# Optimization experiments

Measured on AMD Instinct MI355X. Metric: run time of the kernel, lower is better.

The kernel has to match this reference:

```python
import jax, jax.numpy as jnp
import numpy as np

N, D, C = 2048, 192, 100000
S, M = 30.0, 0.2

def setup_inputs() -> dict:
    key = jax.random.key(0)
    k1, k2, k3 = jax.random.split(key, 3)
    x = jax.random.normal(k1, (N, D), dtype=jnp.float32)
    W = jax.random.normal(k2, (C, D), dtype=jnp.float32) * 0.05
    label = jax.random.randint(k3, (N,), 0, C, dtype=jnp.int64)
    return {"x": x, "W": W, "label": label}

def reference(x, W, label):
    # NOTE: the original torch code's weight-normalization loop is a no-op
    # (it rebinds the local name W, never mutating the parameter), so W is
    # intentionally NOT normalized here; only x is.
    xn = x / jnp.linalg.norm(x, axis=1, keepdims=True)          # [N, D]
    wf = jnp.einsum("nd,cd->nc", xn, W)                          # [N, C]
    tgt = jnp.take_along_axis(wf, label[:, None], axis=1)[:, 0]  # [N]
    numer = S * (tgt - M)                                        # margin-adjusted target logit
    logits = S * wf
    # replace the label column with the margin-adjusted numerator so that
    # logsumexp(logits) == log(exp(numer) + sum_{j!=y} exp(s*wf[:,j]))
    logits = logits.at[jnp.arange(N), label].set(numer)
    L = numer - jax.nn.logsumexp(logits, axis=1)                 # [N]
    return -jnp.mean(L)
```

## Files before the change

### kernel.cpp

```cpp
#include <hip/hip_runtime.h>
#include <stdint.h>


constexpr int N  = 2048;
constexpr int D  = 192;
constexpr int C  = 100000;
constexpr int KT = D / 32;
constexpr int TILE = 512;
constexpr int RT16 = C / 16;
constexpr int TPG = 12;
constexpr int CX = 523;
constexpr int NT16 = CX * TPG;
constexpr float PHANTOM = (float)(NT16 * 16 - C);
constexpr int BANDS = 4;
constexpr int RYB = N / (64 * BANDS);
constexpr int BUF = 4 * KT * TILE;
constexpr int NXB = N / 4;

#define S_SCALE 30.0f
#define MARGIN  0.2f
#define S_LOG2E 43.2808512266689f

using short8 = __attribute__((ext_vector_type(8))) short;
using f32x4  = __attribute__((ext_vector_type(4))) float;

typedef __attribute__((address_space(1))) const void GV;
typedef __attribute__((address_space(3))) void LV;

__device__ inline unsigned short f2bf(float f) {
  unsigned int u = __float_as_uint(f);
  u += 0x7fffu + ((u >> 16) & 1u);
  return (unsigned short)(u >> 16);
}

__device__ inline int pack_idx(int r, int k) {
  return ((r >> 4) * KT + (k >> 5)) * TILE + (((k >> 3) & 3) * 16 + (r & 15)) * 8 + (k & 7);
}

__device__ inline float row_sum16(float v) {
  int x;
  x = __float_as_int(v);
  v += __int_as_float(__builtin_amdgcn_update_dpp(0, x, 0x128, 0xF, 0xF, true));
  x = __float_as_int(v);
  v += __int_as_float(__builtin_amdgcn_update_dpp(0, x, 0x124, 0xF, 0xF, true));
  x = __float_as_int(v);
  v += __int_as_float(__builtin_amdgcn_update_dpp(0, x, 0x04E, 0xF, 0xF, true));
  x = __float_as_int(v);
  v += __int_as_float(__builtin_amdgcn_update_dpp(0, x, 0x0B1, 0xF, 0xF, true));
  return v;
}

__global__ __launch_bounds__(256) void prep_all(
    const float* __restrict__ x, const float* __restrict__ W,
    unsigned short* __restrict__ xnb, unsigned short* __restrict__ Wb,
    float* __restrict__ out) {
  const int bid  = blockIdx.x;
  const int lane = threadIdx.x & 63;
  if (bid == 0 && threadIdx.x == 0) out[0] = 0.0f;

  if (bid < NXB) {
    const int row = bid * 4 + (threadIdx.x >> 6);
    const float* xr = x + (size_t)row * D;
    float v0 = xr[lane], v1 = xr[lane + 64], v2 = xr[lane + 128];
    float ss = v0 * v0 + v1 * v1 + v2 * v2;
#pragma unroll
    for (int off = 32; off > 0; off >>= 1) ss += __shfl_xor(ss, off, 64);
    const float inv = rsqrtf(ss) * S_LOG2E;
    xnb[pack_idx(row, lane)]       = f2bf(v0 * inv);
    xnb[pack_idx(row, lane + 64)]  = f2bf(v1 * inv);
    xnb[pack_idx(row, lane + 128)] = f2bf(v2 * inv);
  } else {
    const int t16 = (bid - NXB) * 4 + (threadIdx.x >> 6);
    const int m = lane & 15, q = lane >> 4;
    unsigned short* dst = Wb + (size_t)t16 * KT * TILE + lane * 8;
    if (t16 < RT16) {
      const float* src = W + (size_t)(t16 * 16 + m) * D + q * 8;
#pragma unroll
      for (int ks = 0; ks < KT; ++ks) {
        const float4* s4 = (const float4*)(src + ks * 32);
        float4 f0 = s4[0], f1 = s4[1];
        short8 hv;
        hv[0] = (short)f2bf(f0.x); hv[1] = (short)f2bf(f0.y);
        hv[2] = (short)f2bf(f0.z); hv[3] = (short)f2bf(f0.w);
        hv[4] = (short)f2bf(f1.x); hv[5] = (short)f2bf(f1.y);
        hv[6] = (short)f2bf(f1.z); hv[7] = (short)f2bf(f1.w);
        *(short8*)(dst + (size_t)ks * TILE) = hv;
      }
    } else {
      const short8 z = {0, 0, 0, 0, 0, 0, 0, 0};
#pragma unroll
      for (int ks = 0; ks < KT; ++ks) *(short8*)(dst + (size_t)ks * TILE) = z;
    }
  }
}

__global__ __launch_bounds__(256, 3) void gemm_lse(
    const unsigned short* __restrict__ xnb,
    const unsigned short* __restrict__ Wb,
    float* __restrict__ partial) {
  __shared__ alignas(16) unsigned short As[2 * BUF];
  __shared__ alignas(16) float rs_lds[4][256];

  const int tid = threadIdx.x;
  const int bid = blockIdx.x;
  const int cx = bid >> 3, ry = bid & 7;

  {
    const unsigned short* slab = xnb + (size_t)(ry * BANDS) * BUF;
#pragma unroll
    for (int i = 0; i < 6; ++i) {
      const int chunk = tid + i * 256;
      __builtin_amdgcn_global_load_lds(
          (GV*)((const char*)slab + (size_t)chunk * 16),
          (LV*)((char*)As + (size_t)chunk * 16), 16, 0, 0);
    }
  }

  const int lane = tid & 63, wave = tid >> 6;
  const int m = lane & 15, quad = lane >> 4;

  short8 breg[3][KT];
#pragma unroll
  for (int tc = 0; tc < 3; ++tc)
#pragma unroll
    for (int ks = 0; ks < KT; ++ks)
      breg[tc][ks] = *(const short8*)(
          Wb + (size_t)((cx * TPG + wave * 3 + tc) * KT + ks) * TILE + lane * 8);

  const f32x4 zero4 = {0.0f, 0.0f, 0.0f, 0.0f};

  for (int b = 0; b < BANDS; ++b) {
    __syncthreads();

    if (b + 1 < BANDS) {
      const unsigned short* slab = xnb + (size_t)(ry * BANDS + b + 1) * BUF;
      char* dst = (char*)&As[((b + 1) & 1) * BUF];
#pragma unroll
      for (int i = 0; i < 6; ++i) {
        const int chunk = tid + i * 256;
        __builtin_amdgcn_global_load_lds(
            (GV*)((const char*)slab + (size_t)chunk * 16),
            (LV*)(dst + (size_t)chunk * 16), 16, 0, 0);
      }
    }

    const unsigned short* Ab = &As[(b & 1) * BUF];

    f32x4 acc[4][3];
#pragma unroll
    for (int a = 0; a < 4; ++a)
#pragma unroll
      for (int c = 0; c < 3; ++c) acc[a][c] = zero4;

#pragma unroll
    for (int ks = 0; ks < KT; ++ks) {
      short8 af[4];
#pragma unroll
      for (int tr = 0; tr < 4; ++tr)
        af[tr] = *(const short8*)(&Ab[(tr * KT + ks) * TILE + lane * 8]);
#pragma unroll
      for (int tr = 0; tr < 4; ++tr)
#pragma unroll
        for (int tc = 0; tc < 3; ++tc)
          acc[tr][tc] = __builtin_amdgcn_mfma_f32_16x16x32_bf16(
              af[tr], breg[tc][ks], acc[tr][tc], 0, 0, 0);
    }

#pragma unroll
    for (int tr = 0; tr < 4; ++tr) {
      float rv0 = 0.f, rv1 = 0.f, rv2 = 0.f, rv3 = 0.f;
#pragma unroll
      for (int tc = 0; tc < 3; ++tc) {
        rv0 += __builtin_amdgcn_exp2f(acc[tr][tc][0]);
        rv1 += __builtin_amdgcn_exp2f(acc[tr][tc][1]);
        rv2 += __builtin_amdgcn_exp2f(acc[tr][tc][2]);
        rv3 += __builtin_amdgcn_exp2f(acc[tr][tc][3]);
      }
      rv0 = row_sum16(rv0);
      rv1 = row_sum16(rv1);
      rv2 = row_sum16(rv2);
      rv3 = row_sum16(rv3);
      if (m == 0) {
        float4 v = make_float4(rv0, rv1, rv2, rv3);
        *(float4*)(&rs_lds[wave][b * 64 + tr * 16 + quad * 4]) = v;
      }
    }
  }

  __syncthreads();
  if (tid < 256) {
    const float s = rs_lds[0][tid] + rs_lds[1][tid] + rs_lds[2][tid] + rs_lds[3][tid];
    partial[(size_t)cx * N + ry * 256 + tid] = s;
  }
}

__global__ __launch_bounds__(256) void finalize_rows(
    const float* __restrict__ x, const float* __restrict__ W,
    const int* __restrict__ label, const float* __restrict__ partial,
    float* __restrict__ out) {
  const int row  = blockIdx.x * 4 + (threadIdx.x >> 6);
  const int lane = threadIdx.x & 63;
  const float* xr = x + (size_t)row * D;
  float v0 = xr[lane], v1 = xr[lane + 64], v2 = xr[lane + 128];
  float ss = v0 * v0 + v1 * v1 + v2 * v2;
  const int lab = label[row];
  const float* wr = W + (size_t)lab * D;
  float d = v0 * wr[lane] + v1 * wr[lane + 64] + v2 * wr[lane + 128];
  float p = 0.0f;
  for (int s = lane; s < CX; s += 64) p += partial[(size_t)s * N + row];
#pragma unroll
  for (int off = 32; off > 0; off >>= 1) {
    ss += __shfl_xor(ss, off, 64);
    d  += __shfl_xor(d,  off, 64);
    p  += __shfl_xor(p,  off, 64);
  }
  __shared__ float part[4];
  if (lane == 0) {
    const float tgt   = d * rsqrtf(ss);
    const float numer = S_SCALE * (tgt - MARGIN);
    const float se = p - PHANTOM - __expf(S_SCALE * tgt) + __expf(numer);
    part[threadIdx.x >> 6] = numer - logf(se);
  }
  __syncthreads();
  if (threadIdx.x == 0) {
    const float blocksum = part[0] + part[1] + part[2] + part[3];
    atomicAdd(out, -blocksum * (1.0f / (float)N));
  }
}

extern "C" void kernel_launch(void* const* d_in, const int* in_sizes, int n_in,
                              void* d_out, int out_size, void* d_ws, size_t ws_size,
                              hipStream_t stream) {
  const float* x     = (const float*)d_in[0];
  const float* W     = (const float*)d_in[1];
  const int*   label = (const int*)d_in[2];
  float*       out   = (float*)d_out;

  char* ws = (char*)d_ws;
  size_t off = 0;
  unsigned short* xnb = (unsigned short*)(ws + off); off += (size_t)N * D * 2;
  unsigned short* Wb  = (unsigned short*)(ws + off); off += (size_t)NT16 * KT * TILE * 2;
  float* partial = (float*)(ws + off); off += (size_t)CX * N * 4;

  prep_all<<<NXB + NT16 / 4, 256, 0, stream>>>(x, W, xnb, Wb, out);

  gemm_lse<<<CX * RYB, 256, 0, stream>>>(xnb, Wb, partial);

  finalize_rows<<<N / 4, 256, 0, stream>>>(x, W, label, partial, out);
}
```

Before: 211.5 us.

## Fuse W bf16 conversion into GEMM kernel, dropping packed W workspace

Removes the W-conversion half of the prep kernel and the packed bf16 W buffer. Each GEMM block now loads its fp32 W rows directly into registers and converts them to bf16 in the MFMA fragment layout, zero-filling phantom tiles. This avoids writing the bf16 copy of W and reading it back. The cost is that each W tile is fetched in fp32 (twice the bytes) by all 8 row-band blocks, which relies on L2/MALL reuse among adjacent blocks, and the conversion is repeated in each of those blocks.

```diff
diff --git a/kernel.cpp b/kernel.cpp
--- a/kernel.cpp
+++ b/kernel.cpp
@@ -50,31 +50,56 @@
   return v;
 }
 
-__global__ __launch_bounds__(256) void prep_all(
-    const float* __restrict__ x, const float* __restrict__ W,
-    unsigned short* __restrict__ xnb, unsigned short* __restrict__ Wb,
+__global__ __launch_bounds__(256) void prep_x(
+    const float* __restrict__ x, unsigned short* __restrict__ xnb,
     float* __restrict__ out) {
   const int bid  = blockIdx.x;
   const int lane = threadIdx.x & 63;
   if (bid == 0 && threadIdx.x == 0) out[0] = 0.0f;
 
-  if (bid < NXB) {
-    const int row = bid * 4 + (threadIdx.x >> 6);
-    const float* xr = x + (size_t)row * D;
-    float v0 = xr[lane], v1 = xr[lane + 64], v2 = xr[lane + 128];
-    float ss = v0 * v0 + v1 * v1 + v2 * v2;
-#pragma unroll
-    for (int off = 32; off > 0; off >>= 1) ss += __shfl_xor(ss, off, 64);
-    const float inv = rsqrtf(ss) * S_LOG2E;
-    xnb[pack_idx(row, lane)]       = f2bf(v0 * inv);
-    xnb[pack_idx(row, lane + 64)]  = f2bf(v1 * inv);
-    xnb[pack_idx(row, lane + 128)] = f2bf(v2 * inv);
-  } else {
-    const int t16 = (bid - NXB) * 4 + (threadIdx.x >> 6);
-    const int m = lane & 15, q = lane >> 4;
-    unsigned short* dst = Wb + (size_t)t16 * KT * TILE + lane * 8;
+  const int row = bid * 4 + (threadIdx.x >> 6);
+  const float* xr = x + (size_t)row * D;
+  float v0 = xr[lane], v1 = xr[lane + 64], v2 = xr[lane + 128];
+  float ss = v0 * v0 + v1 * v1 + v2 * v2;
+#pragma unroll
+  for (int off = 32; off > 0; off >>= 1) ss += __shfl_xor(ss, off, 64);
+  const float inv = rsqrtf(ss) * S_LOG2E;
+  xnb[pack_idx(row, lane)]       = f2bf(v0 * inv);
+  xnb[pack_idx(row, lane + 64)]  = f2bf(v1 * inv);
+  xnb[pack_idx(row, lane + 128)] = f2bf(v2 * inv);
+}
+
+__global__ __launch_bounds__(256, 3) void gemm_lse(
+    const unsigned short* __restrict__ xnb,
+    const float* __restrict__ W,
+    float* __restrict__ partial) {
+  __shared__ alignas(16) unsigned short As[2 * BUF];
+  __shared__ alignas(16) float rs_lds[4][256];
+
+  const int tid = threadIdx.x;
+  const int bid = blockIdx.x;
+  const int cx = bid >> 3, ry = bid & 7;
+
+  {
+    const unsigned short* slab = xnb + (size_t)(ry * BANDS) * BUF;
+#pragma unroll
+    for (int i = 0; i < 6; ++i) {
+      const int chunk = tid + i * 256;
+      __builtin_amdgcn_global_load_lds(
+          (GV*)((const char*)slab + (size_t)chunk * 16),
+          (LV*)((char*)As + (size_t)chunk * 16), 16, 0, 0);
+    }
+  }
+
+  const int lane = tid & 63, wave = tid >> 6;
+  const int m = lane & 15, quad = lane >> 4;
+
+  short8 breg[3][KT];
+#pragma unroll
+  for (int tc = 0; tc < 3; ++tc) {
+    const int t16 = cx * TPG + wave * 3 + tc;
     if (t16 < RT16) {
-      const float* src = W + (size_t)(t16 * 16 + m) * D + q * 8;
+      const float* src = W + (size_t)(t16 * 16 + m) * D + quad * 8;
 #pragma unroll
       for (int ks = 0; ks < KT; ++ks) {
         const float4* s4 = (const float4*)(src + ks * 32);
@@ -84,48 +109,14 @@
         hv[2] = (short)f2bf(f0.z); hv[3] = (short)f2bf(f0.w);
         hv[4] = (short)f2bf(f1.x); hv[5] = (short)f2bf(f1.y);
         hv[6] = (short)f2bf(f1.z); hv[7] = (short)f2bf(f1.w);
-        *(short8*)(dst + (size_t)ks * TILE) = hv;
+        breg[tc][ks] = hv;
       }
     } else {
       const short8 z = {0, 0, 0, 0, 0, 0, 0, 0};
 #pragma unroll
-      for (int ks = 0; ks < KT; ++ks) *(short8*)(dst + (size_t)ks * TILE) = z;
-    }
-  }
-}
-
-__global__ __launch_bounds__(256, 3) void gemm_lse(
-    const unsigned short* __restrict__ xnb,
-    const unsigned short* __restrict__ Wb,
-    float* __restrict__ partial) {
-  __shared__ alignas(16) unsigned short As[2 * BUF];
-  __shared__ alignas(16) float rs_lds[4][256];
-
-  const int tid = threadIdx.x;
-  const int bid = blockIdx.x;
-  const int cx = bid >> 3, ry = bid & 7;
-
-  {
-    const unsigned short* slab = xnb + (size_t)(ry * BANDS) * BUF;
-#pragma unroll
-    for (int i = 0; i < 6; ++i) {
-      const int chunk = tid + i * 256;
-      __builtin_amdgcn_global_load_lds(
-          (GV*)((const char*)slab + (size_t)chunk * 16),
-          (LV*)((char*)As + (size_t)chunk * 16), 16, 0, 0);
-    }
-  }
-
-  const int lane = tid & 63, wave = tid >> 6;
-  const int m = lane & 15, quad = lane >> 4;
-
-  short8 breg[3][KT];
-#pragma unroll
-  for (int tc = 0; tc < 3; ++tc)
-#pragma unroll
-    for (int ks = 0; ks < KT; ++ks)
-      breg[tc][ks] = *(const short8*)(
-          Wb + (size_t)((cx * TPG + wave * 3 + tc) * KT + ks) * TILE + lane * 8);
+      for (int ks = 0; ks < KT; ++ks) breg[tc][ks] = z;
+    }
+  }
 
   const f32x4 zero4 = {0.0f, 0.0f, 0.0f, 0.0f};
 
@@ -239,12 +230,11 @@
   char* ws = (char*)d_ws;
   size_t off = 0;
   unsigned short* xnb = (unsigned short*)(ws + off); off += (size_t)N * D * 2;
-  unsigned short* Wb  = (unsigned short*)(ws + off); off += (size_t)NT16 * KT * TILE * 2;
   float* partial = (float*)(ws + off); off += (size_t)CX * N * 4;
 
-  prep_all<<<NXB + NT16 / 4, 256, 0, stream>>>(x, W, xnb, Wb, out);
-
-  gemm_lse<<<CX * RYB, 256, 0, stream>>>(xnb, Wb, partial);
+  prep_x<<<NXB, 256, 0, stream>>>(x, xnb, out);
+
+  gemm_lse<<<CX * RYB, 256, 0, stream>>>(xnb, W, partial);
 
   finalize_rows<<<N / 4, 256, 0, stream>>>(x, W, label, partial, out);
 }
```

New measurement: 216.2 us. 1.02x slower.

## Replace partial-sum buffer with atomic row sums, remap blocks per XCD, pack bf16

Applied to the files above, without the earlier changes.

The target-logit dot product moves into the prep kernel, and the per-column-block partial array (CX×N floats) is replaced by atomic adds into a single N-length rowsum buffer. The final kernel then only reads two small arrays. The GEMM grid is padded to CXP and remapped so that blocks sharing the same column tile land on the same XCD, which should improve L2 reuse of W tiles. W conversion uses the hardware packed bf16 convert instruction. These changes remove the large partial write and read but add float atomic contention and make the summation order nondeterministic.

```diff
diff --git a/kernel.cpp b/kernel.cpp
--- a/kernel.cpp
+++ b/kernel.cpp
@@ -16,6 +16,7 @@
 constexpr int RYB = N / (64 * BANDS);
 constexpr int BUF = 4 * KT * TILE;
 constexpr int NXB = N / 4;
+constexpr int CXP = 528;
 
 #define S_SCALE 30.0f
 #define MARGIN  0.2f
@@ -33,6 +34,12 @@
   return (unsigned short)(u >> 16);
 }
 
+__device__ inline unsigned int cvtpk(float lo, float hi) {
+  unsigned int r;
+  asm("v_cvt_pk_bf16_f32 %0, %1, %2" : "=v"(r) : "v"(lo), "v"(hi));
+  return r;
+}
+
 __device__ inline int pack_idx(int r, int k) {
   return ((r >> 4) * KT + (k >> 5)) * TILE + (((k >> 3) & 3) * 16 + (r & 15)) * 8 + (k & 7);
 }
@@ -52,7 +59,9 @@
 
 __global__ __launch_bounds__(256) void prep_all(
     const float* __restrict__ x, const float* __restrict__ W,
+    const int* __restrict__ label,
     unsigned short* __restrict__ xnb, unsigned short* __restrict__ Wb,
+    float* __restrict__ aux, float* __restrict__ rowsum,
     float* __restrict__ out) {
   const int bid  = blockIdx.x;
   const int lane = threadIdx.x & 63;
@@ -63,12 +72,23 @@
     const float* xr = x + (size_t)row * D;
     float v0 = xr[lane], v1 = xr[lane + 64], v2 = xr[lane + 128];
     float ss = v0 * v0 + v1 * v1 + v2 * v2;
-#pragma unroll
-    for (int off = 32; off > 0; off >>= 1) ss += __shfl_xor(ss, off, 64);
-    const float inv = rsqrtf(ss) * S_LOG2E;
+    const int lab = label[row];
+    const float* wr = W + (size_t)lab * D;
+    float d = v0 * wr[lane] + v1 * wr[lane + 64] + v2 * wr[lane + 128];
+#pragma unroll
+    for (int off = 32; off > 0; off >>= 1) {
+      ss += __shfl_xor(ss, off, 64);
+      d  += __shfl_xor(d,  off, 64);
+    }
+    const float rinv = rsqrtf(ss);
+    const float inv = rinv * S_LOG2E;
     xnb[pack_idx(row, lane)]       = f2bf(v0 * inv);
     xnb[pack_idx(row, lane + 64)]  = f2bf(v1 * inv);
     xnb[pack_idx(row, lane + 128)] = f2bf(v2 * inv);
+    if (lane == 0) {
+      aux[row]    = d * rinv;
+      rowsum[row] = 0.0f;
+    }
   } else {
     const int t16 = (bid - NXB) * 4 + (threadIdx.x >> 6);
     const int m = lane & 15, q = lane >> 4;
@@ -79,12 +99,12 @@
       for (int ks = 0; ks < KT; ++ks) {
         const float4* s4 = (const float4*)(src + ks * 32);
         float4 f0 = s4[0], f1 = s4[1];
-        short8 hv;
-        hv[0] = (short)f2bf(f0.x); hv[1] = (short)f2bf(f0.y);
-        hv[2] = (short)f2bf(f0.z); hv[3] = (short)f2bf(f0.w);
-        hv[4] = (short)f2bf(f1.x); hv[5] = (short)f2bf(f1.y);
-        hv[6] = (short)f2bf(f1.z); hv[7] = (short)f2bf(f1.w);
-        *(short8*)(dst + (size_t)ks * TILE) = hv;
+        union { uint4 u; short8 s; } cv;
+        cv.u.x = cvtpk(f0.x, f0.y);
+        cv.u.y = cvtpk(f0.z, f0.w);
+        cv.u.z = cvtpk(f1.x, f1.y);
+        cv.u.w = cvtpk(f1.z, f1.w);
+        *(short8*)(dst + (size_t)ks * TILE) = cv.s;
       }
     } else {
       const short8 z = {0, 0, 0, 0, 0, 0, 0, 0};
@@ -97,13 +117,16 @@
 __global__ __launch_bounds__(256, 3) void gemm_lse(
     const unsigned short* __restrict__ xnb,
     const unsigned short* __restrict__ Wb,
-    float* __restrict__ partial) {
+    float* __restrict__ rowsum) {
   __shared__ alignas(16) unsigned short As[2 * BUF];
   __shared__ alignas(16) float rs_lds[4][256];
 
   const int tid = threadIdx.x;
   const int bid = blockIdx.x;
-  const int cx = bid >> 3, ry = bid & 7;
+  const int xcd = bid & 7, j = bid >> 3;
+  const int ry = j & 7;
+  const int cx = (j >> 3) * 8 + xcd;
+  if (cx >= CX) return;
 
   {
     const unsigned short* slab = xnb + (size_t)(ry * BANDS) * BUF;
@@ -188,39 +211,23 @@
   }
 
   __syncthreads();
-  if (tid < 256) {
-    const float s = rs_lds[0][tid] + rs_lds[1][tid] + rs_lds[2][tid] + rs_lds[3][tid];
-    partial[(size_t)cx * N + ry * 256 + tid] = s;
-  }
-}
-
-__global__ __launch_bounds__(256) void finalize_rows(
-    const float* __restrict__ x, const float* __restrict__ W,
-    const int* __restrict__ label, const float* __restrict__ partial,
+  const float s = rs_lds[0][tid] + rs_lds[1][tid] + rs_lds[2][tid] + rs_lds[3][tid];
+  atomicAdd(&rowsum[ry * 256 + tid], s);
+}
+
+__global__ __launch_bounds__(256) void finalize_tiny(
+    const float* __restrict__ aux, const float* __restrict__ rowsum,
     float* __restrict__ out) {
-  const int row  = blockIdx.x * 4 + (threadIdx.x >> 6);
-  const int lane = threadIdx.x & 63;
-  const float* xr = x + (size_t)row * D;
-  float v0 = xr[lane], v1 = xr[lane + 64], v2 = xr[lane + 128];
-  float ss = v0 * v0 + v1 * v1 + v2 * v2;
-  const int lab = label[row];
-  const float* wr = W + (size_t)lab * D;
-  float d = v0 * wr[lane] + v1 * wr[lane + 64] + v2 * wr[lane + 128];
-  float p = 0.0f;
-  for (int s = lane; s < CX; s += 64) p += partial[(size_t)s * N + row];
-#pragma unroll
-  for (int off = 32; off > 0; off >>= 1) {
-    ss += __shfl_xor(ss, off, 64);
-    d  += __shfl_xor(d,  off, 64);
-    p  += __shfl_xor(p,  off, 64);
-  }
+  const int row  = blockIdx.x * 256 + threadIdx.x;
+  const int lane = threadIdx.x & 63, wave = threadIdx.x >> 6;
+  const float tgt   = aux[row];
+  const float numer = S_SCALE * (tgt - MARGIN);
+  const float se = rowsum[row] - PHANTOM - __expf(S_SCALE * tgt) + __expf(numer);
+  float L = numer - logf(se);
+#pragma unroll
+  for (int off = 32; off > 0; off >>= 1) L += __shfl_xor(L, off, 64);
   __shared__ float part[4];
-  if (lane == 0) {
-    const float tgt   = d * rsqrtf(ss);
-    const float numer = S_SCALE * (tgt - MARGIN);
-    const float se = p - PHANTOM - __expf(S_SCALE * tgt) + __expf(numer);
-    part[threadIdx.x >> 6] = numer - logf(se);
-  }
+  if (lane == 0) part[wave] = L;
   __syncthreads();
   if (threadIdx.x == 0) {
     const float blocksum = part[0] + part[1] + part[2] + part[3];
@@ -240,11 +247,12 @@
   size_t off = 0;
   unsigned short* xnb = (unsigned short*)(ws + off); off += (size_t)N * D * 2;
   unsigned short* Wb  = (unsigned short*)(ws + off); off += (size_t)NT16 * KT * TILE * 2;
-  float* partial = (float*)(ws + off); off += (size_t)CX * N * 4;
-
-  prep_all<<<NXB + NT16 / 4, 256, 0, stream>>>(x, W, xnb, Wb, out);
-
-  gemm_lse<<<CX * RYB, 256, 0, stream>>>(xnb, Wb, partial);
-
-  finalize_rows<<<N / 4, 256, 0, stream>>>(x, W, label, partial, out);
-}
+  float* aux    = (float*)(ws + off); off += (size_t)N * 4;
+  float* rowsum = (float*)(ws + off); off += (size_t)N * 4;
+
+  prep_all<<<NXB + NT16 / 4, 256, 0, stream>>>(x, W, label, xnb, Wb, aux, rowsum, out);
+
+  gemm_lse<<<CXP * RYB, 256, 0, stream>>>(xnb, Wb, rowsum);
+
+  finalize_tiny<<<N / 256, 256, 0, stream>>>(aux, rowsum, out);
+}
```

Result: faster. 203.9 us (-3.6%).
